# Kernel optimization log

Hardware: AMD Instinct MI355X
Metric: run time of the kernel (lower is better)

## Reference

```python
import jax, jax.numpy as jnp
import numpy as np

B, D_IN, HID, DEPTH = 16384, 128, 16, 8
N_INNER = 2 ** DEPTH - 1   # 255
N_LEAF = 2 ** DEPTH        # 256


def setup_inputs() -> dict:
    key = jax.random.key(0)
    ks = jax.random.split(key, 4)
    x = jax.random.normal(ks[0], (B, D_IN), jnp.float32)
    # Batched per-inner-node tiny MLP parameters (PyTorch stores one Sequential per node;
    # we stack them along a leading node axis so the math is identical but vectorized).
    W1 = jax.random.normal(ks[1], (N_INNER, D_IN, HID), jnp.float32) / np.sqrt(D_IN).astype(np.float32)
    b1 = jnp.zeros((N_INNER, HID), jnp.float32)
    W2 = jax.random.normal(ks[2], (N_INNER, HID), jnp.float32) / np.sqrt(HID).astype(np.float32)
    b2 = jnp.zeros((N_INNER,), jnp.float32)
    leaf = jax.random.normal(ks[3], (N_LEAF, 1), jnp.float32) * 0.1
    return {"x": x, "W1": W1, "b1": b1, "W2": W2, "b2": b2, "leaf": leaf}


def reference(x, W1, b1, W2, b2, leaf):
    b = x.shape[0]
    depth = int(np.log2(leaf.shape[0]))
    # All inner-node gates in one batched GEMM: p[b, n] = sigmoid(W2_n . relu(W1_n^T x_b + b1_n) + b2_n)
    h1 = jax.nn.relu(jnp.einsum('bi,nih->bnh', x, W1) + b1[None])  # [B, N_inner, hid]
    p = jax.nn.sigmoid(jnp.einsum('bnh,nh->bn', h1, W2) + b2[None])  # [B, N_inner]

    # Level-by-level probability propagation (heap-ordered nodes):
    # children of node j are 2j+1 (left, mass*(1-p)) and 2j+2 (right, mass*p).
    r = jnp.ones((b, 1), x.dtype)
    levels = []
    for l in range(depth):
        levels.append(r)
        pl = p[:, 2 ** l - 1: 2 ** (l + 1) - 1]  # probs of nodes at level l, [B, 2^l]
        # interleave (left, right) so child ordering matches heap indexing
        r = jnp.stack([r * (1.0 - pl), r * pl], axis=-1).reshape(b, 2 ** (l + 1))
    node_reach = jnp.concatenate(levels, axis=1)  # [B, N_inner]
    path_probs = r                                 # [B, N_leaf]

    h = (path_probs @ leaf)[:, 0]                  # [B]
    return (h, path_probs, p, node_reach)
```

## Files before the change

### kernel.cpp

```cpp
#include <hip/hip_runtime.h>

#define BATCH 16384
#define DIN   128
#define HIDN  16
#define NNODE 255
#define NLEAF 256
#define TR    16

typedef _Float16 half8 __attribute__((ext_vector_type(8)));
typedef _Float16 half4 __attribute__((ext_vector_type(4)));
typedef float   float4v __attribute__((ext_vector_type(4)));

__global__ __launch_bounds__(256) void k_pack(const float* __restrict__ x, const float* __restrict__ w1,
                                              const float* __restrict__ w2,
                                              half8* __restrict__ xp, half8* __restrict__ w1p,
                                              _Float16* __restrict__ w2h) {
    __shared__ float w[DIN * 17];
    int t = threadIdx.x;
    if (blockIdx.x < 1024) {
        int gid  = blockIdx.x * 256 + t;
        int lane = gid & 63;
        int kc   = (gid >> 6) & 3;
        int bt   = gid >> 8;
        const float4* src = (const float4*)(x + (size_t)(bt * 16 + (lane & 15)) * DIN + kc * 32 + ((lane >> 4) * 8));
        float4 v0 = src[0], v1 = src[1];
        half8 v;
        v[0] = (_Float16)v0.x; v[1] = (_Float16)v0.y; v[2] = (_Float16)v0.z; v[3] = (_Float16)v0.w;
        v[4] = (_Float16)v1.x; v[5] = (_Float16)v1.y; v[6] = (_Float16)v1.z; v[7] = (_Float16)v1.w;
        xp[gid] = v;
    } else {
        int n = blockIdx.x - 1024;
        const float4* src = (const float4*)(w1 + (size_t)n * (DIN * HIDN)) + t * 2;
        float4 a0 = src[0], a1 = src[1];
        int base = t * 8;
#pragma unroll
        for (int e = 0; e < 4; ++e) {
            int idx0 = base + e, idx1 = base + 4 + e;
            w[(idx0 >> 4) * 17 + (idx0 & 15)] = (&a0.x)[e];
            w[(idx1 >> 4) * 17 + (idx1 & 15)] = (&a1.x)[e];
        }
        __syncthreads();
        int L  = t & 63;
        int kc = t >> 6;
        int m  = L & 15;
        int k0 = kc * 32 + (L >> 4) * 8;
        half8 v;
#pragma unroll
        for (int j = 0; j < 8; ++j) v[j] = (_Float16)w[(k0 + j) * 17 + m];
        w1p[(size_t)n * 256 + t] = v;
        if (t < HIDN) w2h[n * HIDN + t] = (_Float16)w2[n * HIDN + t];
    }
}

__global__ __launch_bounds__(256, 4) void k_mlp(const half8* __restrict__ xp, const half8* __restrict__ w1p,
                                                const float* __restrict__ b1, const _Float16* __restrict__ w2h,
                                                const float* __restrict__ b2, float* __restrict__ p_ws) {
    int wv   = threadIdx.x >> 6;
    int lane = threadIdx.x & 63;
    int q    = lane >> 4;
    int bt0  = blockIdx.x * 16 + wv * 4;
    int n0   = blockIdx.y * 15;

    half8 bq[4][4];
#pragma unroll
    for (int t = 0; t < 4; ++t)
#pragma unroll
        for (int kc = 0; kc < 4; ++kc)
            bq[t][kc] = xp[(size_t)((bt0 + t) * 4 + kc) * 64 + lane];
    asm volatile("" ::: "memory");

    for (int i = 0; i < 15; ++i) {
        int n = n0 + i;
        half8 a[4];
#pragma unroll
        for (int kc = 0; kc < 4; ++kc) a[kc] = w1p[(size_t)(n * 4 + kc) * 64 + lane];
        float4 b1f = ((const float4*)(b1 + n * HIDN))[q];
        half4  a2  = *(const half4*)(w2h + n * HIDN + q * 4);
        float  b2v = b2[n];
#pragma unroll
        for (int t = 0; t < 4; ++t) {
            float4v acc = {b1f.x, b1f.y, b1f.z, b1f.w};
#pragma unroll
            for (int kc = 0; kc < 4; ++kc)
                acc = __builtin_amdgcn_mfma_f32_16x16x32_f16(a[kc], bq[t][kc], acc, 0, 0, 0);
            half4 rb;
#pragma unroll
            for (int r = 0; r < 4; ++r) rb[r] = (_Float16)fmaxf(acc[r], 0.f);
            float4v acc2 = {b2v, b2v, b2v, b2v};
            acc2 = __builtin_amdgcn_mfma_f32_16x16x16f16(a2, rb, acc2, 0, 0, 0);
            if (lane < 16)
                p_ws[(size_t)n * BATCH + (bt0 + t) * 16 + lane] = acc2[0];
        }
    }
}

__global__ __launch_bounds__(256) void k_tree(const float* __restrict__ p_ws, const float* __restrict__ leaf,
                                              float* __restrict__ h_out, float* __restrict__ pp_out,
                                              float* __restrict__ p_out, float* __restrict__ nr_out) {
    __shared__ float sp[TR][NNODE + 2];
    int wv   = threadIdx.x >> 6;
    int lane = threadIdx.x & 63;
    int b0   = blockIdx.x * TR;
    int t    = threadIdx.x;

#pragma unroll
    for (int i = 0; i < 16; ++i) {
        int idx = i * 256 + t;
        if (idx < NNODE * TR) {
            int n = idx >> 4, bl = idx & 15;
            float lg = p_ws[(size_t)n * BATCH + b0 + bl];
            sp[bl][n] = __builtin_amdgcn_rcpf(1.f + __builtin_amdgcn_exp2f(-1.44269504088896f * lg));
        }
    }
    __syncthreads();

    for (int r = 0; r < TR; ++r)
        if (t < NNODE)
            p_out[(size_t)(b0 + r) * NNODE + t] = sp[r][t];

    for (int rr = 0; rr < 4; ++rr) {
        int i = wv * 4 + rr;
        int b = b0 + i;
        const float* P = &sp[i][0];
        float* nr = nr_out + (size_t)b * NNODE;

        float pref = 1.f;
#pragma unroll
        for (int l = 0; l < 6; ++l) {
            if ((lane & ((1 << (6 - l)) - 1)) == 0) nr[(1 << l) - 1 + (lane >> (6 - l))] = pref;
            float pv  = P[(1 << l) - 1 + (lane >> (6 - l))];
            int  bit  = (lane >> (5 - l)) & 1;
            pref *= bit ? pv : (1.f - pv);
        }
        nr[63 + lane] = pref;
        float p6 = P[63 + lane];
        float pl = pref * (1.f - p6);
        float pr = pref * p6;
        nr[127 + 2 * lane] = pl;
        nr[128 + 2 * lane] = pr;
        float p7a = P[127 + 2 * lane];
        float p7b = P[128 + 2 * lane];
        float4 pp;
        pp.x = pl * (1.f - p7a);
        pp.y = pl * p7a;
        pp.z = pr * (1.f - p7b);
        pp.w = pr * p7b;
        *(float4*)(pp_out + (size_t)b * NLEAF + 4 * lane) = pp;
        const float4 lf = *(const float4*)(leaf + 4 * lane);
        float hs = pp.x * lf.x + pp.y * lf.y + pp.z * lf.z + pp.w * lf.w;
#pragma unroll
        for (int off = 1; off < 64; off <<= 1) hs += __shfl_xor(hs, off, 64);
        if (lane == 0) h_out[b] = hs;
    }
}

extern "C" void kernel_launch(void* const* d_in, const int* in_sizes, int n_in,
                              void* d_out, int out_size, void* d_ws, size_t ws_size,
                              hipStream_t stream) {
    const float* x    = (const float*)d_in[0];
    const float* W1   = (const float*)d_in[1];
    const float* b1   = (const float*)d_in[2];
    const float* W2   = (const float*)d_in[3];
    const float* b2   = (const float*)d_in[4];
    const float* leaf = (const float*)d_in[5];

    float* out    = (float*)d_out;
    float* h_out  = out;
    float* pp_out = out + BATCH;
    float* p_out  = pp_out + (size_t)BATCH * NLEAF;
    float* nr_out = p_out + (size_t)BATCH * NNODE;

    half8*    xp   = (half8*)d_ws;
    half8*    w1p  = xp + (size_t)1024 * 4 * 64;
    _Float16* w2h  = (_Float16*)(w1p + (size_t)NNODE * 256);
    float*    p_ws = (float*)((char*)w2h + ((NNODE * HIDN * 2 + 255) & ~255));

    hipLaunchKernelGGL(k_pack, dim3(1024 + NNODE), dim3(256), 0, stream, x, W1, W2, xp, w1p, w2h);
    hipLaunchKernelGGL(k_mlp,  dim3(64, 17), dim3(256), 0, stream, xp, w1p, b1, w2h, b2, p_ws);
    hipLaunchKernelGGL(k_tree, dim3(BATCH / TR), dim3(256), 0, stream,
                       p_ws, leaf, h_out, pp_out, p_out, nr_out);
}
```

Baseline: 123.3 us.

## Prefetch next node weights, move sigmoid into MLP, vectorize tree loads, nontemporal stores

In the MLP kernel, the next node's W1, b1, W2 and b2 are software-prefetched while the current node's MFMAs run, and the launch-bounds occupancy hint drops from 4 to 3 to leave room for the extra registers. The sigmoid moves from the tree kernel into the MLP epilogue. The tree kernel now reads p_ws with float4 loads instead of scalar loads, and all large output writes use nontemporal stores to avoid polluting the cache. The prefetch adds register pressure and lowers occupancy, which could offset the latency hiding.

```diff
diff --git a/kernel.cpp b/kernel.cpp
--- a/kernel.cpp
+++ b/kernel.cpp
@@ -52,7 +52,7 @@
     }
 }
 
-__global__ __launch_bounds__(256, 4) void k_mlp(const half8* __restrict__ xp, const half8* __restrict__ w1p,
+__global__ __launch_bounds__(256, 3) void k_mlp(const half8* __restrict__ xp, const half8* __restrict__ w1p,
                                                 const float* __restrict__ b1, const _Float16* __restrict__ w2h,
                                                 const float* __restrict__ b2, float* __restrict__ p_ws) {
     int wv   = threadIdx.x >> 6;
@@ -69,14 +69,23 @@
             bq[t][kc] = xp[(size_t)((bt0 + t) * 4 + kc) * 64 + lane];
     asm volatile("" ::: "memory");
 
+    half8 a[4];
+#pragma unroll
+    for (int kc = 0; kc < 4; ++kc) a[kc] = w1p[(size_t)(n0 * 4 + kc) * 64 + lane];
+    float4 b1f = ((const float4*)(b1 + n0 * HIDN))[q];
+    half4  a2  = *(const half4*)(w2h + n0 * HIDN + q * 4);
+    float  b2v = b2[n0];
+
     for (int i = 0; i < 15; ++i) {
-        int n = n0 + i;
-        half8 a[4];
+        int n  = n0 + i;
+        int nn = n + (i < 14 ? 1 : 0);
+        half8 an[4];
 #pragma unroll
-        for (int kc = 0; kc < 4; ++kc) a[kc] = w1p[(size_t)(n * 4 + kc) * 64 + lane];
-        float4 b1f = ((const float4*)(b1 + n * HIDN))[q];
-        half4  a2  = *(const half4*)(w2h + n * HIDN + q * 4);
-        float  b2v = b2[n];
+        for (int kc = 0; kc < 4; ++kc) an[kc] = w1p[(size_t)(nn * 4 + kc) * 64 + lane];
+        float4 b1n = ((const float4*)(b1 + nn * HIDN))[q];
+        half4  a2n = *(const half4*)(w2h + nn * HIDN + q * 4);
+        float  b2n = b2[nn];
+
 #pragma unroll
         for (int t = 0; t < 4; ++t) {
             float4v acc = {b1f.x, b1f.y, b1f.z, b1f.w};
@@ -88,9 +97,14 @@
             for (int r = 0; r < 4; ++r) rb[r] = (_Float16)fmaxf(acc[r], 0.f);
             float4v acc2 = {b2v, b2v, b2v, b2v};
             acc2 = __builtin_amdgcn_mfma_f32_16x16x16f16(a2, rb, acc2, 0, 0, 0);
-            if (lane < 16)
-                p_ws[(size_t)n * BATCH + (bt0 + t) * 16 + lane] = acc2[0];
+            if (lane < 16) {
+                float sg = __builtin_amdgcn_rcpf(1.f + __builtin_amdgcn_exp2f(-1.44269504088896f * acc2[0]));
+                p_ws[(size_t)n * BATCH + (bt0 + t) * 16 + lane] = sg;
+            }
         }
+#pragma unroll
+        for (int kc = 0; kc < 4; ++kc) a[kc] = an[kc];
+        b1f = b1n; a2 = a2n; b2v = b2n;
     }
 }
 
@@ -104,19 +118,19 @@
     int t    = threadIdx.x;
 
 #pragma unroll
-    for (int i = 0; i < 16; ++i) {
+    for (int i = 0; i < 4; ++i) {
         int idx = i * 256 + t;
-        if (idx < NNODE * TR) {
-            int n = idx >> 4, bl = idx & 15;
-            float lg = p_ws[(size_t)n * BATCH + b0 + bl];
-            sp[bl][n] = __builtin_amdgcn_rcpf(1.f + __builtin_amdgcn_exp2f(-1.44269504088896f * lg));
+        if (idx < NNODE * 4) {
+            int n = idx >> 2, b4 = (idx & 3) * 4;
+            const float4 v = *(const float4*)(p_ws + (size_t)n * BATCH + b0 + b4);
+            sp[b4 + 0][n] = v.x; sp[b4 + 1][n] = v.y; sp[b4 + 2][n] = v.z; sp[b4 + 3][n] = v.w;
         }
     }
     __syncthreads();
 
     for (int r = 0; r < TR; ++r)
         if (t < NNODE)
-            p_out[(size_t)(b0 + r) * NNODE + t] = sp[r][t];
+            __builtin_nontemporal_store(sp[r][t], &p_out[(size_t)(b0 + r) * NNODE + t]);
 
     for (int rr = 0; rr < 4; ++rr) {
         int i = wv * 4 + rr;
@@ -127,17 +141,18 @@
         float pref = 1.f;
 #pragma unroll
         for (int l = 0; l < 6; ++l) {
-            if ((lane & ((1 << (6 - l)) - 1)) == 0) nr[(1 << l) - 1 + (lane >> (6 - l))] = pref;
+            if ((lane & ((1 << (6 - l)) - 1)) == 0)
+                __builtin_nontemporal_store(pref, &nr[(1 << l) - 1 + (lane >> (6 - l))]);
             float pv  = P[(1 << l) - 1 + (lane >> (6 - l))];
             int  bit  = (lane >> (5 - l)) & 1;
             pref *= bit ? pv : (1.f - pv);
         }
-        nr[63 + lane] = pref;
+        __builtin_nontemporal_store(pref, &nr[63 + lane]);
         float p6 = P[63 + lane];
         float pl = pref * (1.f - p6);
         float pr = pref * p6;
-        nr[127 + 2 * lane] = pl;
-        nr[128 + 2 * lane] = pr;
+        __builtin_nontemporal_store(pl, &nr[127 + 2 * lane]);
+        __builtin_nontemporal_store(pr, &nr[128 + 2 * lane]);
         float p7a = P[127 + 2 * lane];
         float p7b = P[128 + 2 * lane];
         float4 pp;
@@ -145,7 +160,8 @@
         pp.y = pl * p7a;
         pp.z = pr * (1.f - p7b);
         pp.w = pr * p7b;
-        *(float4*)(pp_out + (size_t)b * NLEAF + 4 * lane) = pp;
+        float4v ppv = {pp.x, pp.y, pp.z, pp.w};
+        __builtin_nontemporal_store(ppv, (float4v*)(pp_out + (size_t)b * NLEAF + 4 * lane));
         const float4 lf = *(const float4*)(leaf + 4 * lane);
         float hs = pp.x * lf.x + pp.y * lf.y + pp.z * lf.z + pp.w * lf.w;
 #pragma unroll
```

Result: slower. 130.2 us (+5.6%).
